# Kernel optimization log

Hardware: AMD Instinct MI355X
Metric: run time of the kernel (lower is better)

The kernel has to match this reference:

```python
import jax, jax.numpy as jnp
import numpy as np

# fHOG orientation lookup (cos/sin of k*20 degrees), exactly the hardcoded
# constants used in Felzenszwalb's features.cc / mmcv extract_hog kernel.
UU = jnp.array([1.0000, 0.9397, 0.7660, 0.5000, 0.1736,
                -0.1736, -0.5000, -0.7660, -0.9397], dtype=jnp.float32)
VV = jnp.array([0.0000, 0.3420, 0.6428, 0.8660, 0.9848,
                0.9848, 0.8660, 0.6428, 0.3420], dtype=jnp.float32)
EPS = 1e-4


def _hog(img, sbin):
    B, C, H, W = img.shape
    bh = int(round(H / sbin)); bw = int(round(W / sbin))
    vh, vw = bh * sbin, bw * sbin
    # central differences at pixels (1..visible-2), source index clamped to dim-2
    ys = jnp.clip(jnp.arange(1, vh - 1), 0, H - 2)
    xs = jnp.clip(jnp.arange(1, vw - 1), 0, W - 2)
    dy = img[:, :, ys + 1][:, :, :, xs] - img[:, :, ys - 1][:, :, :, xs]
    dx = img[:, :, ys][:, :, :, xs + 1] - img[:, :, ys][:, :, :, xs - 1]
    v = dx * dx + dy * dy                      # [B,3,hg,wg]
    ch = jnp.argmax(v, axis=1, keepdims=True)  # channel with max gradient energy
    dxs = jnp.take_along_axis(dx, ch, axis=1)[:, 0]
    dys = jnp.take_along_axis(dy, ch, axis=1)[:, 0]
    mag = jnp.sqrt(dxs * dxs + dys * dys)      # [B,hg,wg]
    # snap to one of 18 signed orientations
    dot = UU[None, :, None, None] * dxs[:, None] + VV[None, :, None, None] * dys[:, None]
    best_o = jnp.argmax(jnp.concatenate([dot, -dot], axis=1), axis=1)  # [B,hg,wg]
    # bilinear spatial soft-binning into sbin x sbin cells
    yp = (jnp.arange(1, vh - 1, dtype=img.dtype) + 0.5) / sbin - 0.5
    xp = (jnp.arange(1, vw - 1, dtype=img.dtype) + 0.5) / sbin - 0.5
    iyp = jnp.floor(yp).astype(jnp.int32); ixp = jnp.floor(xp).astype(jnp.int32)
    vy0 = yp - iyp; vx0 = xp - ixp; vy1 = 1.0 - vy0; vx1 = 1.0 - vx0
    hg, wg = vh - 2, vw - 2
    bidx = jnp.arange(B)[:, None, None]
    IY = jnp.broadcast_to(iyp[None, :, None], (B, hg, wg))
    IX = jnp.broadcast_to(ixp[None, None, :], (B, hg, wg))
    WY0 = vy0[None, :, None]; WY1 = vy1[None, :, None]
    WX0 = vx0[None, None, :]; WX1 = vx1[None, None, :]
    hist = jnp.zeros((B, 18, bh, bw), dtype=img.dtype)

    def scat(h, iy, ix, w):
        valid = (iy >= 0) & (iy < bh) & (ix >= 0) & (ix < bw)
        iyc = jnp.clip(iy, 0, bh - 1); ixc = jnp.clip(ix, 0, bw - 1)
        return h.at[bidx, best_o, iyc, ixc].add(jnp.where(valid, w * mag, 0.0))

    hist = scat(hist, IY, IX, WY1 * WX1)
    hist = scat(hist, IY, IX + 1, WY1 * WX0)
    hist = scat(hist, IY + 1, IX, WY0 * WX1)
    hist = scat(hist, IY + 1, IX + 1, WY0 * WX0)
    # cell energy from contrast-insensitive sums
    s = hist[:, :9] + hist[:, 9:]
    norm = jnp.sum(s * s, axis=1)              # [B,bh,bw]
    # 2x2 block sums of norm
    T = norm[:, :-1, :-1] + norm[:, 1:, :-1] + norm[:, :-1, 1:] + norm[:, 1:, 1:]
    n1 = jax.lax.rsqrt(T[:, 1:, 1:] + EPS)[:, None]
    n2 = jax.lax.rsqrt(T[:, :-1, 1:] + EPS)[:, None]
    n3 = jax.lax.rsqrt(T[:, 1:, :-1] + EPS)[:, None]
    n4 = jax.lax.rsqrt(T[:, :-1, :-1] + EPS)[:, None]
    src = hist[:, :, 1:-1, 1:-1]               # [B,18,oh,ow]
    h1 = jnp.minimum(src * n1, 0.2); h2 = jnp.minimum(src * n2, 0.2)
    h3 = jnp.minimum(src * n3, 0.2); h4 = jnp.minimum(src * n4, 0.2)
    f_cs = 0.5 * (h1 + h2 + h3 + h4)           # 18 contrast-sensitive feats
    ss = src[:, :9] + src[:, 9:]
    f_ci = 0.5 * (jnp.minimum(ss * n1, 0.2) + jnp.minimum(ss * n2, 0.2)
                  + jnp.minimum(ss * n3, 0.2) + jnp.minimum(ss * n4, 0.2))
    tex = 0.2357 * jnp.stack([h1.sum(1), h2.sum(1), h3.sum(1), h4.sum(1)], axis=1)
    feat = jnp.concatenate([f_cs, f_ci, tex], axis=1)  # [B,31,oh,ow]
    return jnp.pad(feat, ((0, 0), (0, 0), (1, 1), (1, 1)))


def setup_inputs() -> dict:
    key = jax.random.key(0)
    img = jax.random.uniform(key, (16, 3, 512, 512), dtype=jnp.float32)
    return {"input": img, "sbin": 4}


def reference(input, sbin):
    return _hog(input, sbin)
```

## Files before the change

### kernel.cpp

```cpp
#include <hip/hip_runtime.h>
#include <hip/hip_fp16.h>

#define BATCH 16
#define H 512
#define W 512
#define BH 128
#define BW 128
#define HG 510
#define WG 510
#define PKW 512


__global__ __launch_bounds__(256) void hog_grad(const float* __restrict__ img,
                                                unsigned int* __restrict__ pk)
{
    int gx = blockIdx.x * 64 + threadIdx.x;
    int qy = blockIdx.y * 4 + threadIdx.y;
    int b  = blockIdx.z;
    int x0 = gx * 4;
    int y0 = qy * 4;
    bool edge = (x0 < 508);

    const float* im = img + (size_t)b * 3 * H * W;

    float bv[16], bx[16], by[16];
#pragma unroll
    for (int i = 0; i < 16; i++) { bv[i] = -1.f; bx[i] = 0.f; by[i] = 0.f; }

#pragma unroll
    for (int c = 0; c < 3; c++) {
        const float* base = im + (size_t)c * H * W;
        float Wr[6][6];
#pragma unroll
        for (int j = 0; j < 6; j++) {
            int pr = y0 + j; if (pr > 511) pr = 511;
            const float* rowp = base + (size_t)pr * W + x0;
            float4 a = *(const float4*)rowp;
            Wr[j][0] = a.x; Wr[j][1] = a.y; Wr[j][2] = a.z; Wr[j][3] = a.w;
            if (j >= 1 && j <= 4) {
                if (edge || pr < 511) {
                    float2 f = *(const float2*)(rowp + 4);
                    Wr[j][4] = f.x; Wr[j][5] = f.y;
                } else { Wr[j][4] = 0.f; Wr[j][5] = 0.f; }
            } else {
                Wr[j][4] = edge ? rowp[4] : 0.0f;
                Wr[j][5] = 0.f;
            }
        }
#pragma unroll
        for (int r = 0; r < 4; r++) {
#pragma unroll
            for (int i = 0; i < 4; i++) {
                float dx = __fsub_rn(Wr[r + 1][i + 2], Wr[r + 1][i]);
                float dy = __fsub_rn(Wr[r + 2][i + 1], Wr[r][i + 1]);
                float v = __fadd_rn(__fmul_rn(dx, dx), __fmul_rn(dy, dy));
                int k = r * 4 + i;
                if (v > bv[k]) { bv[k] = v; bx[k] = dx; by[k] = dy; }
            }
        }
    }

    const float uu[9] = {1.0f, 0.9397f, 0.766f, 0.5f, 0.1736f, -0.1736f, -0.5f, -0.766f, -0.9397f};
    const float vv[9] = {0.0f, 0.342f, 0.6428f, 0.866f, 0.9848f, 0.9848f, 0.866f, 0.6428f, 0.342f};

#pragma unroll
    for (int r = 0; r < 4; r++) {
        int y = y0 + r;
        if (y >= HG) break;
        unsigned int pkv[4];
#pragma unroll
        for (int i = 0; i < 4; i++) {
            int k = r * 4 + i;
            float mg = __fsqrt_rn(bv[k]);
            float d[9];
#pragma unroll
            for (int o = 0; o < 9; o++)
                d[o] = __fadd_rn(__fmul_rn(uu[o], bx[k]), __fmul_rn(vv[o], by[k]));
            float best = -1e30f; int bo = 0;
#pragma unroll
            for (int o = 0; o < 9; o++) { if (d[o] > best) { best = d[o]; bo = o; } }
#pragma unroll
            for (int o = 0; o < 9; o++) { float nd = -d[o]; if (nd > best) { best = nd; bo = o + 9; } }
            unsigned int v = (__float_as_uint(mg) & 0xFFFFFFE0u) | (unsigned int)bo;
            pkv[i] = (x0 + i < WG) ? v : 0u;
        }
        uint4 o4 = make_uint4(pkv[0], pkv[1], pkv[2], pkv[3]);
        *(uint4*)(pk + ((size_t)b * HG + y) * PKW + x0) = o4;
    }
}

__global__ __launch_bounds__(256) void hog_hist(const unsigned int* __restrict__ pk,
                                                __half2* __restrict__ hist,
                                                float* __restrict__ nrm)
{
    __shared__ float hl0[18 * 256];
    __shared__ float hl1[18 * 256];
    int cx = threadIdx.x;
    int cy = blockIdx.y * 2 + threadIdx.y;
    int b = blockIdx.z;
    int t = threadIdx.y * 128 + cx;

#pragma unroll
    for (int o = 0; o < 18; o++) { hl0[o * 256 + t] = 0.0f; hl1[o * 256 + t] = 0.0f; }

    const float wt[8] = {0.125f, 0.375f, 0.625f, 0.875f, 0.875f, 0.625f, 0.375f, 0.125f};
    const float wl[4] = {0.0f, 0.125f, 0.375f, 0.625f};
    const float wm[4] = {0.875f, 0.875f, 0.625f, 0.375f};

    const unsigned int* pb = pk + (size_t)b * HG * PKW;
    int ry0 = 4 * cy - 3;
    int xb = 4 * cx;

#pragma unroll
    for (int ky = 0; ky < 8; ky++) {
        int ry = ry0 + ky;
        if ((unsigned)ry >= (unsigned)HG) continue;
        float wy = wt[ky];
        const unsigned int* row = pb + (size_t)ry * PKW;
        if (cx > 0) {
            uint4 L = *(const uint4*)(row + xb - 4);
            { unsigned p = L.y; hl0[(p & 31u) * 256 + t] += (wy * wl[1]) * __uint_as_float(p & 0xFFFFFFE0u); }
            { unsigned p = L.z; hl1[(p & 31u) * 256 + t] += (wy * wl[2]) * __uint_as_float(p & 0xFFFFFFE0u); }
            { unsigned p = L.w; hl0[(p & 31u) * 256 + t] += (wy * wl[3]) * __uint_as_float(p & 0xFFFFFFE0u); }
        }
        uint4 M = *(const uint4*)(row + xb);
        { unsigned p = M.x; hl1[(p & 31u) * 256 + t] += (wy * wm[0]) * __uint_as_float(p & 0xFFFFFFE0u); }
        { unsigned p = M.y; hl0[(p & 31u) * 256 + t] += (wy * wm[1]) * __uint_as_float(p & 0xFFFFFFE0u); }
        if (cx < 127) {
            { unsigned p = M.z; hl1[(p & 31u) * 256 + t] += (wy * wm[2]) * __uint_as_float(p & 0xFFFFFFE0u); }
            { unsigned p = M.w; hl0[(p & 31u) * 256 + t] += (wy * wm[3]) * __uint_as_float(p & 0xFFFFFFE0u); }
            unsigned p = row[xb + 4];
            hl1[(p & 31u) * 256 + t] += (wy * 0.125f) * __uint_as_float(p & 0xFFFFFFE0u);
        }
    }

    float s = 0.0f;
#pragma unroll
    for (int o = 0; o < 9; o++) {
        float lo = hl0[o * 256 + t] + hl1[o * 256 + t];
        float hi = hl0[(o + 9) * 256 + t] + hl1[(o + 9) * 256 + t];
        hist[(((size_t)b * 9 + o) * BH + cy) * BW + cx] = __floats2half2_rn(lo, hi);
        float ss = lo + hi;
        s += ss * ss;
    }
    nrm[((size_t)b * BH + cy) * BW + cx] = s;
}

__global__ __launch_bounds__(256) void hog_feat(const __half2* __restrict__ hist,
                                                const float* __restrict__ nrm,
                                                float* __restrict__ out)
{
    int ox = threadIdx.x;
    int oy = blockIdx.y * 2 + threadIdx.y;
    int b = blockIdx.z;

    if (ox == 0 || ox == BW - 1 || oy == 0 || oy == BH - 1) {
#pragma unroll
        for (int c = 0; c < 31; c++)
            out[(((size_t)b * 31 + c) * BH + oy) * BW + ox] = 0.0f;
        return;
    }

    const float* nb = nrm + (size_t)b * BH * BW;
    float n00 = nb[(size_t)(oy - 1) * BW + ox - 1], n01 = nb[(size_t)(oy - 1) * BW + ox], n02 = nb[(size_t)(oy - 1) * BW + ox + 1];
    float n10 = nb[(size_t)oy * BW + ox - 1],       n11 = nb[(size_t)oy * BW + ox],       n12 = nb[(size_t)oy * BW + ox + 1];
    float n20 = nb[(size_t)(oy + 1) * BW + ox - 1], n21 = nb[(size_t)(oy + 1) * BW + ox], n22 = nb[(size_t)(oy + 1) * BW + ox + 1];

    float T11 = n11 + n21 + n12 + n22;
    float T01 = n01 + n11 + n02 + n12;
    float T10 = n10 + n20 + n11 + n21;
    float T00 = n00 + n10 + n01 + n11;
    float v1 = 1.0f / __fsqrt_rn(T11 + 1e-4f);
    float v2 = 1.0f / __fsqrt_rn(T01 + 1e-4f);
    float v3 = 1.0f / __fsqrt_rn(T10 + 1e-4f);
    float v4 = 1.0f / __fsqrt_rn(T00 + 1e-4f);

    float h[18];
#pragma unroll
    for (int o = 0; o < 9; o++) {
        float2 f = __half22float2(hist[(((size_t)b * 9 + o) * BH + oy) * BW + ox]);
        h[o] = f.x; h[o + 9] = f.y;
    }

    float t1 = 0.f, t2 = 0.f, t3 = 0.f, t4 = 0.f;
#pragma unroll
    for (int o = 0; o < 18; o++) {
        float s = h[o];
        float a1 = fminf(s * v1, 0.2f);
        float a2 = fminf(s * v2, 0.2f);
        float a3 = fminf(s * v3, 0.2f);
        float a4 = fminf(s * v4, 0.2f);
        out[(((size_t)b * 31 + o) * BH + oy) * BW + ox] = 0.5f * (a1 + a2 + a3 + a4);
        t1 += a1; t2 += a2; t3 += a3; t4 += a4;
    }
#pragma unroll
    for (int o = 0; o < 9; o++) {
        float ss = h[o] + h[o + 9];
        float a1 = fminf(ss * v1, 0.2f);
        float a2 = fminf(ss * v2, 0.2f);
        float a3 = fminf(ss * v3, 0.2f);
        float a4 = fminf(ss * v4, 0.2f);
        out[(((size_t)b * 31 + 18 + o) * BH + oy) * BW + ox] = 0.5f * (a1 + a2 + a3 + a4);
    }
    out[(((size_t)b * 31 + 27) * BH + oy) * BW + ox] = 0.2357f * t1;
    out[(((size_t)b * 31 + 28) * BH + oy) * BW + ox] = 0.2357f * t2;
    out[(((size_t)b * 31 + 29) * BH + oy) * BW + ox] = 0.2357f * t3;
    out[(((size_t)b * 31 + 30) * BH + oy) * BW + ox] = 0.2357f * t4;
}

extern "C" void kernel_launch(void* const* d_in, const int* in_sizes, int n_in,
                              void* d_out, int out_size, void* d_ws, size_t ws_size,
                              hipStream_t stream)
{
    const float* img = (const float*)d_in[0];
    float* out = (float*)d_out;
    char* ws = (char*)d_ws;

    unsigned int* pk = (unsigned int*)ws;
    __half2* hist    = (__half2*)(ws + 16715776);
    float* nrm       = (float*)(ws + 26152960);

    dim3 b1(64, 4, 1), g1(2, 32, BATCH);
    hog_grad<<<g1, b1, 0, stream>>>(img, pk);

    dim3 b2(128, 2, 1), g2(1, BH / 2, BATCH);
    hog_hist<<<g2, b2, 0, stream>>>(pk, hist, nrm);
    hog_feat<<<g2, b2, 0, stream>>>(hist, nrm, out);
}
```

Before: 118.8 us.

## Use half2 LDS histogram accumulators and vectorize feature kernel to four cells per thread

The histogram kernel now accumulates orientation bins in packed half2 shared memory instead of two fp32 arrays of 18 bins, halving LDS footprint and the final combine work. The feature kernel processes four adjacent cells per thread, loading hist as uint4 and writing outputs as float4, with a new 32x8 block shape and masked border columns. This is meant to cut LDS pressure and memory transaction counts, at the cost of fp16 accumulation error in the histogram and extra register use.

```diff
diff --git a/kernel.cpp b/kernel.cpp
--- a/kernel.cpp
+++ b/kernel.cpp
@@ -93,15 +93,16 @@
                                                 __half2* __restrict__ hist,
                                                 float* __restrict__ nrm)
 {
-    __shared__ float hl0[18 * 256];
-    __shared__ float hl1[18 * 256];
+    __shared__ __half2 hl0[9 * 256];
+    __shared__ __half2 hl1[9 * 256];
     int cx = threadIdx.x;
     int cy = blockIdx.y * 2 + threadIdx.y;
     int b = blockIdx.z;
     int t = threadIdx.y * 128 + cx;
 
-#pragma unroll
-    for (int o = 0; o < 18; o++) { hl0[o * 256 + t] = 0.0f; hl1[o * 256 + t] = 0.0f; }
+    const __half2 z2 = __halves2half2(__ushort_as_half(0), __ushort_as_half(0));
+#pragma unroll
+    for (int o = 0; o < 9; o++) { hl0[o * 256 + t] = z2; hl1[o * 256 + t] = z2; }
 
     const float wt[8] = {0.125f, 0.375f, 0.625f, 0.875f, 0.875f, 0.625f, 0.375f, 0.125f};
     const float wl[4] = {0.0f, 0.125f, 0.375f, 0.625f};
@@ -110,6 +111,13 @@
     const unsigned int* pb = pk + (size_t)b * HG * PKW;
     int ry0 = 4 * cy - 3;
     int xb = 4 * cx;
+
+#define ACC(B, P, WW) { unsigned _p = (P); unsigned _o = _p & 31u;                         \
+        __half _hv = __float2half((WW) * __uint_as_float(_p & 0xFFFFFFE0u));               \
+        bool _lo = _o < 9u; unsigned _o9 = _lo ? _o : _o - 9u;                             \
+        __half2 _ad = _lo ? __halves2half2(_hv, __ushort_as_half(0))                       \
+                          : __halves2half2(__ushort_as_half(0), _hv);                      \
+        B[_o9 * 256 + t] = __hadd2(B[_o9 * 256 + t], _ad); }
 
 #pragma unroll
     for (int ky = 0; ky < 8; ky++) {
@@ -119,28 +127,28 @@
         const unsigned int* row = pb + (size_t)ry * PKW;
         if (cx > 0) {
             uint4 L = *(const uint4*)(row + xb - 4);
-            { unsigned p = L.y; hl0[(p & 31u) * 256 + t] += (wy * wl[1]) * __uint_as_float(p & 0xFFFFFFE0u); }
-            { unsigned p = L.z; hl1[(p & 31u) * 256 + t] += (wy * wl[2]) * __uint_as_float(p & 0xFFFFFFE0u); }
-            { unsigned p = L.w; hl0[(p & 31u) * 256 + t] += (wy * wl[3]) * __uint_as_float(p & 0xFFFFFFE0u); }
+            ACC(hl0, L.y, wy * wl[1]);
+            ACC(hl1, L.z, wy * wl[2]);
+            ACC(hl0, L.w, wy * wl[3]);
         }
         uint4 M = *(const uint4*)(row + xb);
-        { unsigned p = M.x; hl1[(p & 31u) * 256 + t] += (wy * wm[0]) * __uint_as_float(p & 0xFFFFFFE0u); }
-        { unsigned p = M.y; hl0[(p & 31u) * 256 + t] += (wy * wm[1]) * __uint_as_float(p & 0xFFFFFFE0u); }
+        ACC(hl1, M.x, wy * wm[0]);
+        ACC(hl0, M.y, wy * wm[1]);
         if (cx < 127) {
-            { unsigned p = M.z; hl1[(p & 31u) * 256 + t] += (wy * wm[2]) * __uint_as_float(p & 0xFFFFFFE0u); }
-            { unsigned p = M.w; hl0[(p & 31u) * 256 + t] += (wy * wm[3]) * __uint_as_float(p & 0xFFFFFFE0u); }
-            unsigned p = row[xb + 4];
-            hl1[(p & 31u) * 256 + t] += (wy * 0.125f) * __uint_as_float(p & 0xFFFFFFE0u);
-        }
-    }
+            ACC(hl1, M.z, wy * wm[2]);
+            ACC(hl0, M.w, wy * wm[3]);
+            ACC(hl1, row[xb + 4], wy * 0.125f);
+        }
+    }
+#undef ACC
 
     float s = 0.0f;
 #pragma unroll
     for (int o = 0; o < 9; o++) {
-        float lo = hl0[o * 256 + t] + hl1[o * 256 + t];
-        float hi = hl0[(o + 9) * 256 + t] + hl1[(o + 9) * 256 + t];
-        hist[(((size_t)b * 9 + o) * BH + cy) * BW + cx] = __floats2half2_rn(lo, hi);
-        float ss = lo + hi;
+        __half2 hh = __hadd2(hl0[o * 256 + t], hl1[o * 256 + t]);
+        hist[(((size_t)b * 9 + o) * BH + cy) * BW + cx] = hh;
+        float2 f = __half22float2(hh);
+        float ss = f.x + f.y;
         s += ss * ss;
     }
     nrm[((size_t)b * BH + cy) * BW + cx] = s;
@@ -150,62 +158,104 @@
                                                 const float* __restrict__ nrm,
                                                 float* __restrict__ out)
 {
-    int ox = threadIdx.x;
-    int oy = blockIdx.y * 2 + threadIdx.y;
-    int b = blockIdx.z;
-
-    if (ox == 0 || ox == BW - 1 || oy == 0 || oy == BH - 1) {
+    int tx = threadIdx.x;
+    int oy = blockIdx.y * 8 + threadIdx.y;
+    int b  = blockIdx.z;
+    int cx0 = tx * 4;
+
+    if (oy == 0 || oy == BH - 1) {
+        float4 z4 = make_float4(0.f, 0.f, 0.f, 0.f);
 #pragma unroll
         for (int c = 0; c < 31; c++)
-            out[(((size_t)b * 31 + c) * BH + oy) * BW + ox] = 0.0f;
+            *(float4*)(out + (((size_t)b * 31 + c) * BH + oy) * BW + cx0) = z4;
         return;
     }
 
-    const float* nb = nrm + (size_t)b * BH * BW;
-    float n00 = nb[(size_t)(oy - 1) * BW + ox - 1], n01 = nb[(size_t)(oy - 1) * BW + ox], n02 = nb[(size_t)(oy - 1) * BW + ox + 1];
-    float n10 = nb[(size_t)oy * BW + ox - 1],       n11 = nb[(size_t)oy * BW + ox],       n12 = nb[(size_t)oy * BW + ox + 1];
-    float n20 = nb[(size_t)(oy + 1) * BW + ox - 1], n21 = nb[(size_t)(oy + 1) * BW + ox], n22 = nb[(size_t)(oy + 1) * BW + ox + 1];
-
-    float T11 = n11 + n21 + n12 + n22;
-    float T01 = n01 + n11 + n02 + n12;
-    float T10 = n10 + n20 + n11 + n21;
-    float T00 = n00 + n10 + n01 + n11;
-    float v1 = 1.0f / __fsqrt_rn(T11 + 1e-4f);
-    float v2 = 1.0f / __fsqrt_rn(T01 + 1e-4f);
-    float v3 = 1.0f / __fsqrt_rn(T10 + 1e-4f);
-    float v4 = 1.0f / __fsqrt_rn(T00 + 1e-4f);
-
-    float h[18];
+    float v1[4], v2[4], v3[4], v4[4];
+    {
+        const float* nb = nrm + (size_t)b * BH * BW;
+        float nn[3][6];
+#pragma unroll
+        for (int r = 0; r < 3; r++) {
+            const float* rp = nb + (size_t)(oy - 1 + r) * BW + cx0;
+#pragma unroll
+            for (int j = 0; j < 6; j++) nn[r][j] = rp[j - 1];
+        }
+#pragma unroll
+        for (int i = 0; i < 4; i++) {
+            float T11 = nn[1][i+1] + nn[2][i+1] + nn[1][i+2] + nn[2][i+2];
+            float T01 = nn[0][i+1] + nn[1][i+1] + nn[0][i+2] + nn[1][i+2];
+            float T10 = nn[1][i]   + nn[2][i]   + nn[1][i+1] + nn[2][i+1];
+            float T00 = nn[0][i]   + nn[1][i]   + nn[0][i+1] + nn[1][i+1];
+            v1[i] = 1.0f / __fsqrt_rn(T11 + 1e-4f);
+            v2[i] = 1.0f / __fsqrt_rn(T01 + 1e-4f);
+            v3[i] = 1.0f / __fsqrt_rn(T10 + 1e-4f);
+            v4[i] = 1.0f / __fsqrt_rn(T00 + 1e-4f);
+        }
+    }
+
+    float h[4][18];
 #pragma unroll
     for (int o = 0; o < 9; o++) {
-        float2 f = __half22float2(hist[(((size_t)b * 9 + o) * BH + oy) * BW + ox]);
-        h[o] = f.x; h[o + 9] = f.y;
-    }
-
-    float t1 = 0.f, t2 = 0.f, t3 = 0.f, t4 = 0.f;
+        uint4 q = *(const uint4*)(hist + (((size_t)b * 9 + o) * BH + oy) * BW + cx0);
+        unsigned vs[4] = {q.x, q.y, q.z, q.w};
+#pragma unroll
+        for (int i = 0; i < 4; i++) {
+            float2 f = __half22float2(*(__half2*)&vs[i]);
+            h[i][o] = f.x; h[i][o + 9] = f.y;
+        }
+    }
+
+    bool msk[4];
+#pragma unroll
+    for (int i = 0; i < 4; i++) { int cxi = cx0 + i; msk[i] = (cxi >= 1 && cxi <= 126); }
+
+    float t1[4] = {0,0,0,0}, t2[4] = {0,0,0,0}, t3[4] = {0,0,0,0}, t4[4] = {0,0,0,0};
+    float* ob = out + ((size_t)b * 31) * BH * BW + (size_t)oy * BW + cx0;
+
 #pragma unroll
     for (int o = 0; o < 18; o++) {
-        float s = h[o];
-        float a1 = fminf(s * v1, 0.2f);
-        float a2 = fminf(s * v2, 0.2f);
-        float a3 = fminf(s * v3, 0.2f);
-        float a4 = fminf(s * v4, 0.2f);
-        out[(((size_t)b * 31 + o) * BH + oy) * BW + ox] = 0.5f * (a1 + a2 + a3 + a4);
-        t1 += a1; t2 += a2; t3 += a3; t4 += a4;
+        float st[4];
+#pragma unroll
+        for (int i = 0; i < 4; i++) {
+            float s = h[i][o];
+            float a1 = fminf(s * v1[i], 0.2f);
+            float a2 = fminf(s * v2[i], 0.2f);
+            float a3 = fminf(s * v3[i], 0.2f);
+            float a4 = fminf(s * v4[i], 0.2f);
+            t1[i] += a1; t2[i] += a2; t3[i] += a3; t4[i] += a4;
+            st[i] = msk[i] ? 0.5f * (a1 + a2 + a3 + a4) : 0.f;
+        }
+        *(float4*)(ob + (size_t)o * BH * BW) = make_float4(st[0], st[1], st[2], st[3]);
     }
 #pragma unroll
     for (int o = 0; o < 9; o++) {
-        float ss = h[o] + h[o + 9];
-        float a1 = fminf(ss * v1, 0.2f);
-        float a2 = fminf(ss * v2, 0.2f);
-        float a3 = fminf(ss * v3, 0.2f);
-        float a4 = fminf(ss * v4, 0.2f);
-        out[(((size_t)b * 31 + 18 + o) * BH + oy) * BW + ox] = 0.5f * (a1 + a2 + a3 + a4);
-    }
-    out[(((size_t)b * 31 + 27) * BH + oy) * BW + ox] = 0.2357f * t1;
-    out[(((size_t)b * 31 + 28) * BH + oy) * BW + ox] = 0.2357f * t2;
-    out[(((size_t)b * 31 + 29) * BH + oy) * BW + ox] = 0.2357f * t3;
-    out[(((size_t)b * 31 + 30) * BH + oy) * BW + ox] = 0.2357f * t4;
+        float st[4];
+#pragma unroll
+        for (int i = 0; i < 4; i++) {
+            float ss = h[i][o] + h[i][o + 9];
+            float a1 = fminf(ss * v1[i], 0.2f);
+            float a2 = fminf(ss * v2[i], 0.2f);
+            float a3 = fminf(ss * v3[i], 0.2f);
+            float a4 = fminf(ss * v4[i], 0.2f);
+            st[i] = msk[i] ? 0.5f * (a1 + a2 + a3 + a4) : 0.f;
+        }
+        *(float4*)(ob + (size_t)(18 + o) * BH * BW) = make_float4(st[0], st[1], st[2], st[3]);
+    }
+    {
+        float s1[4], s2[4], s3[4], s4[4];
+#pragma unroll
+        for (int i = 0; i < 4; i++) {
+            s1[i] = msk[i] ? 0.2357f * t1[i] : 0.f;
+            s2[i] = msk[i] ? 0.2357f * t2[i] : 0.f;
+            s3[i] = msk[i] ? 0.2357f * t3[i] : 0.f;
+            s4[i] = msk[i] ? 0.2357f * t4[i] : 0.f;
+        }
+        *(float4*)(ob + (size_t)27 * BH * BW) = make_float4(s1[0], s1[1], s1[2], s1[3]);
+        *(float4*)(ob + (size_t)28 * BH * BW) = make_float4(s2[0], s2[1], s2[2], s2[3]);
+        *(float4*)(ob + (size_t)29 * BH * BW) = make_float4(s3[0], s3[1], s3[2], s3[3]);
+        *(float4*)(ob + (size_t)30 * BH * BW) = make_float4(s4[0], s4[1], s4[2], s4[3]);
+    }
 }
 
 extern "C" void kernel_launch(void* const* d_in, const int* in_sizes, int n_in,
@@ -225,5 +275,7 @@
 
     dim3 b2(128, 2, 1), g2(1, BH / 2, BATCH);
     hog_hist<<<g2, b2, 0, stream>>>(pk, hist, nrm);
-    hog_feat<<<g2, b2, 0, stream>>>(hist, nrm, out);
-}
+
+    dim3 b3(32, 8, 1), g3(1, BH / 8, BATCH);
+    hog_feat<<<g3, b3, 0, stream>>>(hist, nrm, out);
+}
```

Measured after the change: 119.9 us. Within noise of the previous version (+0.9%).
